# Performance work log

Hardware: AMD Instinct MI355X
Metric: run time of the kernel (lower is better)

Reference implementation:

```python
import jax, jax.numpy as jnp
import numpy as np

REF_GROUND_RES = 0.2  # reference_ground_resolution
PR_MIN = 0.2          # pr_min


def setup_inputs() -> dict:
    key = jax.random.key(0)
    k1, k2, k3, k4 = jax.random.split(key, 4)
    B, H, W, N = 8, 512, 512, 128
    pred_hm = jax.random.normal(k1, (B, 1, H, W), dtype=jnp.float32)
    pred_sm = jax.random.normal(k2, (B, 1, H, W), dtype=jnp.float32)
    # per-sample ground resolution in [0.1, 0.5] (avoid divide-by-zero)
    ground_resolution = jax.random.uniform(k3, (B,), dtype=jnp.float32) * 0.4 + 0.1
    mask = jnp.ones((B, 1, H, W), dtype=jnp.float32)
    centers = jax.random.randint(k4, (B, N, 2), 0, H, dtype=jnp.int32)
    return {"pred_hm": pred_hm, "pred_sm": pred_sm,
            "ground_resolution": ground_resolution, "mask": mask,
            "centers": centers}


def _draw_gaussian_broadcast(H, W, centers_f, sigmas):
    # centers_f: [N,2] float (row, col); sigmas: [N]
    yy = jnp.arange(H, dtype=centers_f.dtype)
    xx = jnp.arange(W, dtype=centers_f.dtype)
    dy2 = (yy[None, :] - centers_f[:, 0:1]) ** 2            # [N,H]
    dx2 = (xx[None, :] - centers_f[:, 1:2]) ** 2            # [N,W]
    d2 = dy2[:, :, None] + dx2[:, None, :]                   # [N,H,W]
    g = jnp.exp(-d2 / (2.0 * (sigmas[:, None, None] ** 2)))  # per-center gaussian
    return jnp.max(g, axis=0)                                 # [H,W] max-splat


def reference(pred_hm, pred_sm, ground_resolution, mask, centers):
    B, _, H, W = pred_hm.shape

    def per_sample(hm, sm, c, gr, m):
        sm0 = sm[0]                                # [H,W]
        scale_loss = jnp.mean(sm0 ** 2)
        c = jnp.clip(c, 0, H - 1)                   # clamp like torch.clamp(..., max=H-1)
        # predicted per-center sigma from scale map at the center locations
        sizes = PR_MIN / gr + jax.nn.relu(sm0[c[:, 0], c[:, 1]]) * REF_GROUND_RES / gr
        gt = _draw_gaussian_broadcast(H, W, c.astype(hm.dtype), sizes)
        hm_loss = jnp.mean((hm[0] - gt) ** 2 * m[0])
        return scale_loss, hm_loss, gt

    sl, hl, gts = jax.vmap(per_sample)(pred_hm, pred_sm, centers,
                                       ground_resolution, mask)
    return jnp.mean(sl), jnp.mean(hl), gts[:, None, :, :]
```

## Files before the change

kernel.cpp:

```cpp
#include <hip/hip_runtime.h>

#define HH 512
#define WW 512
#define NB 8
#define NC 128
#define TS 64
#define NTILES 64
#define NBLK (NB * NTILES)
#define CUT 30.0f


__global__ __launch_bounds__(512) void ahl_main_kernel(
    const float* __restrict__ pred_hm,
    const float* __restrict__ pred_sm,
    const float* __restrict__ mask,
    const float* __restrict__ ground_res,
    const int*   __restrict__ centers,
    float* __restrict__ out,
    float2* __restrict__ partials) {
    __shared__ float4 sc[NC];
    __shared__ int s_cnt;
    __shared__ float redS[8];
    __shared__ float redH[8];

    const int b    = blockIdx.x >> 6;
    const int tile = blockIdx.x & 63;
    const int tx0  = (tile & 7) * TS;
    const int ty0  = (tile >> 3) * TS;
    const int tid  = threadIdx.x;

    const int cg  = tid & 15;
    const int r0  = tid >> 4;
    const int x0  = tx0 + cg * 4;
    const int ya  = ty0 + r0;
    const int yb  = ya + 32;

    const size_t sbase = (size_t)b * (HH * WW);
    const size_t ia    = sbase + (size_t)ya * WW + x0;
    const size_t ib    = sbase + (size_t)yb * WW + x0;
    float4 hmA = *(const float4*)&pred_hm[ia];
    float4 smA = *(const float4*)&pred_sm[ia];
    float4 mkA = *(const float4*)&mask[ia];
    float4 hmB = *(const float4*)&pred_hm[ib];
    float4 smB = *(const float4*)&pred_sm[ib];
    float4 mkB = *(const float4*)&mask[ib];

    if (tid < 64) {
        const int lane = tid;
        const unsigned long long below = (1ull << lane) - 1ull;
        const float g    = ground_res[b];
        const float base = 0.2f / g;

        int2 c0 = *(const int2*)&centers[(b * NC + lane) * 2];
        int2 c1 = *(const int2*)&centers[(b * NC + lane + 64) * 2];

        float4 P0, P1;
        bool k0, k1;
        {
            int cy = min(max(c0.x, 0), HH - 1);
            int cx = min(max(c0.y, 0), WW - 1);
            float smv  = pred_sm[sbase + (size_t)cy * WW + cx];
            float size = base * (1.0f + fmaxf(smv, 0.0f));
            float s    = 0.70710678f / size;
            P0 = make_float4(s, -(float)cx * s, -(float)cy * s, 0.0f);
            float a0 = fmaf((float)tx0,            P0.x, P0.y);
            float a1 = fmaf((float)(tx0 + TS - 1), P0.x, P0.y);
            float b0 = fmaf((float)ty0,            P0.x, P0.z);
            float b1 = fmaf((float)(ty0 + TS - 1), P0.x, P0.z);
            float dx = fmaxf(0.0f, fmaxf(a0, -a1));
            float dy = fmaxf(0.0f, fmaxf(b0, -b1));
            k0 = fmaf(dx, dx, dy * dy) < CUT;
        }
        {
            int cy = min(max(c1.x, 0), HH - 1);
            int cx = min(max(c1.y, 0), WW - 1);
            float smv  = pred_sm[sbase + (size_t)cy * WW + cx];
            float size = base * (1.0f + fmaxf(smv, 0.0f));
            float s    = 0.70710678f / size;
            P1 = make_float4(s, -(float)cx * s, -(float)cy * s, 0.0f);
            float a0 = fmaf((float)tx0,            P1.x, P1.y);
            float a1 = fmaf((float)(tx0 + TS - 1), P1.x, P1.y);
            float b0 = fmaf((float)ty0,            P1.x, P1.z);
            float b1 = fmaf((float)(ty0 + TS - 1), P1.x, P1.z);
            float dx = fmaxf(0.0f, fmaxf(a0, -a1));
            float dy = fmaxf(0.0f, fmaxf(b0, -b1));
            k1 = fmaf(dx, dx, dy * dy) < CUT;
        }

        unsigned long long m0 = __ballot(k0);
        if (k0) sc[__popcll(m0 & below)] = P0;
        int base1 = __popcll(m0);
        unsigned long long m1 = __ballot(k1);
        if (k1) sc[base1 + __popcll(m1 & below)] = P1;
        if (lane == 0) s_cnt = base1 + __popcll(m1);
    }
    __syncthreads();
    const int cnt = s_cnt;

    const float yfa = (float)ya;
    const float yfb = (float)yb;
    float xf[4];
#pragma unroll
    for (int j = 0; j < 4; j++) xf[j] = (float)(x0 + j);
    float mA[4] = {1e30f, 1e30f, 1e30f, 1e30f};
    float mB[4] = {1e30f, 1e30f, 1e30f, 1e30f};

    for (int i = 0; i < cnt; i++) {
        float4 P = sc[i];
        float da = fmaf(yfa, P.x, P.z); da *= da;
        float db = fmaf(yfb, P.x, P.z); db *= db;
#pragma unroll
        for (int j = 0; j < 4; j++) {
            float d  = fmaf(xf[j], P.x, P.y);
            float dd = d * d;
            mA[j] = fminf(mA[j], dd + da);
            mB[j] = fminf(mB[j], dd + db);
        }
    }

    float gA0 = __expf(-mA[0]), gA1 = __expf(-mA[1]);
    float gA2 = __expf(-mA[2]), gA3 = __expf(-mA[3]);
    float gB0 = __expf(-mB[0]), gB1 = __expf(-mB[1]);
    float gB2 = __expf(-mB[2]), gB3 = __expf(-mB[3]);

    float2* gpA = (float2*)&out[2 + ia];
    gpA[0] = make_float2(gA0, gA1);
    gpA[1] = make_float2(gA2, gA3);
    float2* gpB = (float2*)&out[2 + ib];
    gpB[0] = make_float2(gB0, gB1);
    gpB[1] = make_float2(gB2, gB3);

    float d0 = hmA.x - gA0, d1 = hmA.y - gA1, d2 = hmA.z - gA2, d3 = hmA.w - gA3;
    float lhm = d0 * d0 * mkA.x;
    lhm = fmaf(d1 * d1, mkA.y, lhm);
    lhm = fmaf(d2 * d2, mkA.z, lhm);
    lhm = fmaf(d3 * d3, mkA.w, lhm);
    d0 = hmB.x - gB0; d1 = hmB.y - gB1; d2 = hmB.z - gB2; d3 = hmB.w - gB3;
    lhm = fmaf(d0 * d0, mkB.x, lhm);
    lhm = fmaf(d1 * d1, mkB.y, lhm);
    lhm = fmaf(d2 * d2, mkB.z, lhm);
    lhm = fmaf(d3 * d3, mkB.w, lhm);

    float lsc = smA.x * smA.x;
    lsc = fmaf(smA.y, smA.y, lsc);
    lsc = fmaf(smA.z, smA.z, lsc);
    lsc = fmaf(smA.w, smA.w, lsc);
    lsc = fmaf(smB.x, smB.x, lsc);
    lsc = fmaf(smB.y, smB.y, lsc);
    lsc = fmaf(smB.z, smB.z, lsc);
    lsc = fmaf(smB.w, smB.w, lsc);

#pragma unroll
    for (int off = 32; off > 0; off >>= 1) {
        lhm += __shfl_down(lhm, off);
        lsc += __shfl_down(lsc, off);
    }
    int lane = tid & 63, wid = tid >> 6;
    if (lane == 0) { redS[wid] = lsc; redH[wid] = lhm; }
    __syncthreads();
    if (tid == 0) {
        float ts = 0.0f, th = 0.0f;
#pragma unroll
        for (int w = 0; w < 8; w++) { ts += redS[w]; th += redH[w]; }
        partials[blockIdx.x] = make_float2(ts, th);
    }
}

__global__ __launch_bounds__(256) void ahl_reduce_kernel(
    const float2* __restrict__ partials, float* __restrict__ out) {
    __shared__ float red[8];
    const int tid = threadIdx.x;
    float ts = 0.0f, th = 0.0f;
    for (int s = tid; s < NBLK; s += 256) {
        float2 a = partials[s];
        ts += a.x;
        th += a.y;
    }
#pragma unroll
    for (int off = 32; off > 0; off >>= 1) {
        ts += __shfl_down(ts, off);
        th += __shfl_down(th, off);
    }
    int lane = tid & 63, wid = tid >> 6;
    if (lane == 0) { red[wid] = ts; red[4 + wid] = th; }
    __syncthreads();
    if (tid == 0) {
        const float invc = 1.0f / (float)((size_t)NB * HH * WW);
        out[0] = (red[0] + red[1] + red[2] + red[3]) * invc;
        out[1] = (red[4] + red[5] + red[6] + red[7]) * invc;
    }
}

extern "C" void kernel_launch(void* const* d_in, const int* in_sizes, int n_in,
                              void* d_out, int out_size, void* d_ws, size_t ws_size,
                              hipStream_t stream) {
    const float* pred_hm    = (const float*)d_in[0];
    const float* pred_sm    = (const float*)d_in[1];
    const float* ground_res = (const float*)d_in[2];
    const float* mask       = (const float*)d_in[3];
    const int*   centers    = (const int*)d_in[4];
    float* out = (float*)d_out;
    float2* partials = (float2*)d_ws;

    ahl_main_kernel<<<NBLK, 512, 0, stream>>>(pred_hm, pred_sm, mask,
                                              ground_res, centers, out,
                                              partials);
    ahl_reduce_kernel<<<1, 256, 0, stream>>>(partials, out);
}
```

Before: 83.84 us.

## Tighten gaussian culling cutoff and fold final reduction into cooperative grid sync

Lowers the per-tile culling threshold on squared normalized distance from 30 to 9. Far fewer centers now pass the cull, so the per-pixel min loop does less work, but any Gaussian contribution below about exp(-9) is dropped. Also removes the separate reduction kernel: each block writes its partial sums atomically, then a cooperative grid-wide sync lets block 0 do the final sum. This needs all 512 blocks of 512 threads to be co-resident on the device.

```diff
diff --git a/kernel.cpp b/kernel.cpp
--- a/kernel.cpp
+++ b/kernel.cpp
@@ -1,4 +1,7 @@
 #include <hip/hip_runtime.h>
+#include <hip/hip_cooperative_groups.h>
+
+namespace cg = cooperative_groups;
 
 #define HH 512
 #define WW 512
@@ -7,8 +10,10 @@
 #define TS 64
 #define NTILES 64
 #define NBLK (NB * NTILES)
-#define CUT 30.0f
-
+#define CUT 9.0f
+
+
+union f2u { float2 f; unsigned long long u; };
 
 __global__ __launch_bounds__(512) void ahl_main_kernel(
     const float* __restrict__ pred_hm,
@@ -29,11 +34,11 @@
     const int ty0  = (tile >> 3) * TS;
     const int tid  = threadIdx.x;
 
-    const int cg  = tid & 15;
-    const int r0  = tid >> 4;
-    const int x0  = tx0 + cg * 4;
-    const int ya  = ty0 + r0;
-    const int yb  = ya + 32;
+    const int cg_  = tid & 15;
+    const int r0   = tid >> 4;
+    const int x0   = tx0 + cg_ * 4;
+    const int ya   = ty0 + r0;
+    const int yb   = ya + 32;
 
     const size_t sbase = (size_t)b * (HH * WW);
     const size_t ia    = sbase + (size_t)ya * WW + x0;
@@ -162,32 +167,33 @@
         float ts = 0.0f, th = 0.0f;
 #pragma unroll
         for (int w = 0; w < 8; w++) { ts += redS[w]; th += redH[w]; }
-        partials[blockIdx.x] = make_float2(ts, th);
-    }
-}
-
-__global__ __launch_bounds__(256) void ahl_reduce_kernel(
-    const float2* __restrict__ partials, float* __restrict__ out) {
-    __shared__ float red[8];
-    const int tid = threadIdx.x;
-    float ts = 0.0f, th = 0.0f;
-    for (int s = tid; s < NBLK; s += 256) {
-        float2 a = partials[s];
-        ts += a.x;
-        th += a.y;
-    }
-#pragma unroll
-    for (int off = 32; off > 0; off >>= 1) {
-        ts += __shfl_down(ts, off);
-        th += __shfl_down(th, off);
-    }
-    int lane = tid & 63, wid = tid >> 6;
-    if (lane == 0) { red[wid] = ts; red[4 + wid] = th; }
-    __syncthreads();
-    if (tid == 0) {
-        const float invc = 1.0f / (float)((size_t)NB * HH * WW);
-        out[0] = (red[0] + red[1] + red[2] + red[3]) * invc;
-        out[1] = (red[4] + red[5] + red[6] + red[7]) * invc;
+        f2u v; v.f = make_float2(ts, th);
+        __hip_atomic_store((unsigned long long*)&partials[blockIdx.x], v.u,
+                           __ATOMIC_RELAXED, __HIP_MEMORY_SCOPE_AGENT);
+    }
+
+    cg::this_grid().sync();
+
+    if (blockIdx.x == 0) {
+        f2u v;
+        v.u = __hip_atomic_load((const unsigned long long*)&partials[tid],
+                                __ATOMIC_RELAXED, __HIP_MEMORY_SCOPE_AGENT);
+        float ts = v.f.x, th = v.f.y;
+#pragma unroll
+        for (int off = 32; off > 0; off >>= 1) {
+            ts += __shfl_down(ts, off);
+            th += __shfl_down(th, off);
+        }
+        if (lane == 0) { redS[wid] = ts; redH[wid] = th; }
+        __syncthreads();
+        if (tid == 0) {
+            const float invc = 1.0f / (float)((size_t)NB * HH * WW);
+            float s0 = 0.0f, h0 = 0.0f;
+#pragma unroll
+            for (int w = 0; w < 8; w++) { s0 += redS[w]; h0 += redH[w]; }
+            out[0] = s0 * invc;
+            out[1] = h0 * invc;
+        }
     }
 }
 
@@ -202,8 +208,9 @@
     float* out = (float*)d_out;
     float2* partials = (float2*)d_ws;
 
-    ahl_main_kernel<<<NBLK, 512, 0, stream>>>(pred_hm, pred_sm, mask,
-                                              ground_res, centers, out,
-                                              partials);
-    ahl_reduce_kernel<<<1, 256, 0, stream>>>(partials, out);
+    void* args[] = {(void*)&pred_hm, (void*)&pred_sm, (void*)&mask,
+                    (void*)&ground_res, (void*)&centers, (void*)&out,
+                    (void*)&partials};
+    hipLaunchCooperativeKernel(ahl_main_kernel, dim3(NBLK), dim3(512),
+                               args, 0, stream);
 }
```

Result: slower. 172.3 us (+105.5%).
